# Kernel optimization log

Measured on AMD Instinct MI355X. Metric: run time of the kernel, lower is better.

## Reference

```python
import jax, jax.numpy as jnp
import numpy as np
from jax import lax

T, B, I, H = 512, 64, 1024, 1024
FORGET_BIAS = 1.0


def setup_inputs() -> dict:
    key = jax.random.key(0)
    k1, k2, k3 = jax.random.split(key, 3)
    x = jax.random.normal(k1, (T, B, I), dtype=jnp.float32)
    # xavier-ish init for kernel, scaled normal for recurrent kernel
    kernel = jax.random.normal(k2, (I, 4 * H), dtype=jnp.float32) * (1.0 / np.sqrt(I))
    recurrent_kernel = jax.random.normal(k3, (H, 4 * H), dtype=jnp.float32) * (1.0 / np.sqrt(H))
    bias = jnp.zeros((4 * H,), dtype=jnp.float32)
    bias = bias.at[2 * H:3 * H].set(FORGET_BIAS)  # forget gate bias (haste gate order i,g,f,o)
    return {"x": x, "kernel": kernel, "recurrent_kernel": recurrent_kernel, "bias": bias}


def reference(x, kernel, recurrent_kernel, bias):
    # x: [T, B, I]; haste LSTM, gate order (i, g, f, o); zoneout=0, dropout=0
    t, b, _ = x.shape
    h = recurrent_kernel.shape[0]
    # precompute input projection for all timesteps: [T, B, 4H]
    wx = jnp.einsum('tbi,ij->tbj', x, kernel) + bias

    def step(carry, wx_t):
        h_prev, c_prev = carry
        v = wx_t + h_prev @ recurrent_kernel  # [B, 4H]
        i_g, g_g, f_g, o_g = jnp.split(v, 4, axis=-1)
        i = jax.nn.sigmoid(i_g)
        g = jnp.tanh(g_g)
        f = jax.nn.sigmoid(f_g)
        o = jax.nn.sigmoid(o_g)
        c_new = f * c_prev + i * g
        h_new = o * jnp.tanh(c_new)
        return (h_new, c_new), h_new

    h0 = jnp.zeros((b, h), dtype=x.dtype)
    c0 = jnp.zeros((b, h), dtype=x.dtype)
    (h_last, c_last), output = lax.scan(step, (h0, c0), wx)
    # output: [T, B, H]; state: ([1,B,H], [1,B,H]) matching torch module
    return output, h_last[None], c_last[None]
```

## Files before the change

kernel.cpp:

```cpp
#include <hip/hip_runtime.h>
#include <math.h>

#define T_STEPS 512
#define B_SZ    64
#define I_SZ    1024
#define H_SZ    1024

__device__ __forceinline__ float sigmoidf_(float x) { return 1.0f / (1.0f + expf(-x)); }

#define BM 64
#define BN 128
#define BK 16

__global__ __launch_bounds__(256)
void wx_gemm(const float* __restrict__ X, const float* __restrict__ W,
             const float* __restrict__ bias, float* __restrict__ wx)
{
    __shared__ float As[BK][BM + 4];
    __shared__ float Bs[BK][BN];

    const int tid = threadIdx.x;
    const int tx  = tid & 15;
    const int ty  = tid >> 4;
    const int m0  = blockIdx.y * BM;
    const int n0  = blockIdx.x * BN;

    float acc[4][8] = {};

    const int arow = tid >> 2;
    const int ak   = (tid & 3) * 4;
    const int brow = tid >> 5;
    const int bcol = (tid & 31) * 4;

    const float* Ag = X + (size_t)(m0 + arow) * I_SZ + ak;
    const float* Bg = W + (size_t)brow * 4096 + n0 + bcol;

    for (int k0 = 0; k0 < I_SZ; k0 += BK) {
        float4 av  = *(const float4*)(Ag + k0);
        float4 bv0 = *(const float4*)(Bg + (size_t)k0 * 4096);
        float4 bv1 = *(const float4*)(Bg + (size_t)(k0 + 8) * 4096);
        __syncthreads();
        As[ak + 0][arow] = av.x;
        As[ak + 1][arow] = av.y;
        As[ak + 2][arow] = av.z;
        As[ak + 3][arow] = av.w;
        *(float4*)&Bs[brow][bcol]     = bv0;
        *(float4*)&Bs[brow + 8][bcol] = bv1;
        __syncthreads();
        #pragma unroll
        for (int kk = 0; kk < BK; ++kk) {
            float4 a  = *(const float4*)&As[kk][ty * 4];
            float4 b0 = *(const float4*)&Bs[kk][tx * 8];
            float4 b1 = *(const float4*)&Bs[kk][tx * 8 + 4];
            float aa[4] = {a.x, a.y, a.z, a.w};
            float bb[8] = {b0.x, b0.y, b0.z, b0.w, b1.x, b1.y, b1.z, b1.w};
            #pragma unroll
            for (int i = 0; i < 4; ++i)
                #pragma unroll
                for (int jn = 0; jn < 8; ++jn)
                    acc[i][jn] = fmaf(aa[i], bb[jn], acc[i][jn]);
        }
    }

    float4 bi0 = *(const float4*)(bias + n0 + tx * 8);
    float4 bi1 = *(const float4*)(bias + n0 + tx * 8 + 4);
    float bb[8] = {bi0.x, bi0.y, bi0.z, bi0.w, bi1.x, bi1.y, bi1.z, bi1.w};
    #pragma unroll
    for (int i = 0; i < 4; ++i) {
        float* orow = wx + (size_t)(m0 + ty * 4 + i) * 4096 + n0 + tx * 8;
        float4 s0 = make_float4(acc[i][0] + bb[0], acc[i][1] + bb[1],
                                acc[i][2] + bb[2], acc[i][3] + bb[3]);
        float4 s1 = make_float4(acc[i][4] + bb[4], acc[i][5] + bb[5],
                                acc[i][6] + bb[6], acc[i][7] + bb[7]);
        *(float4*)orow       = s0;
        *(float4*)(orow + 4) = s1;
    }
}

__device__ __forceinline__ void accum_tile(
    const float* __restrict__ vec,
    const float* __restrict__ mat,
    int j0, int tid, int b, int jj,
    float (&vs)[64][66], float (&ms)[64][20],
    float& a0, float& a1, float& a2, float& a3)
{
    const int lb  = tid & 63;
    const int lkq = tid >> 6;
    const int rk  = tid & 63;
    const int rg  = tid >> 6;

    const float* Vg = vec + (size_t)lb * 1024 + lkq * 16;
    const float* Mg = mat + (size_t)rk * 4096 + (size_t)rg * 1024 + j0;

    for (int k0 = 0; k0 < 1024; k0 += 64) {
        float4 v0 = *(const float4*)(Vg + k0 + 0);
        float4 v1 = *(const float4*)(Vg + k0 + 4);
        float4 v2 = *(const float4*)(Vg + k0 + 8);
        float4 v3 = *(const float4*)(Vg + k0 + 12);
        float4 mv = *(const float4*)(Mg + (size_t)k0 * 4096);
        __syncthreads();
        const int kb = lkq * 16;
        vs[kb +  0][lb] = v0.x; vs[kb +  1][lb] = v0.y;
        vs[kb +  2][lb] = v0.z; vs[kb +  3][lb] = v0.w;
        vs[kb +  4][lb] = v1.x; vs[kb +  5][lb] = v1.y;
        vs[kb +  6][lb] = v1.z; vs[kb +  7][lb] = v1.w;
        vs[kb +  8][lb] = v2.x; vs[kb +  9][lb] = v2.y;
        vs[kb + 10][lb] = v2.z; vs[kb + 11][lb] = v2.w;
        vs[kb + 12][lb] = v3.x; vs[kb + 13][lb] = v3.y;
        vs[kb + 14][lb] = v3.z; vs[kb + 15][lb] = v3.w;
        ms[rk][ 0 + rg] = mv.x;
        ms[rk][ 4 + rg] = mv.y;
        ms[rk][ 8 + rg] = mv.z;
        ms[rk][12 + rg] = mv.w;
        __syncthreads();
        #pragma unroll
        for (int kk = 0; kk < 64; ++kk) {
            float hv = vs[kk][b];
            float4 r = *(const float4*)&ms[kk][jj * 4];
            a0 = fmaf(hv, r.x, a0);
            a1 = fmaf(hv, r.y, a1);
            a2 = fmaf(hv, r.z, a2);
            a3 = fmaf(hv, r.w, a3);
        }
    }
}

__global__ __launch_bounds__(256)
void lstm_step(const float* __restrict__ wx_t,
               const float* __restrict__ x_t,
               const float* __restrict__ W,
               const float* __restrict__ bias,
               const float* __restrict__ h_prev,
               const float* __restrict__ R,
               float* __restrict__ h_out,
               float* __restrict__ c_st)
{
    __shared__ float vs[64][66];
    __shared__ float ms[64][20];

    const int tid = threadIdx.x;
    const int b   = tid & 63;
    const int jj  = tid >> 6;
    const int j0  = blockIdx.x * 4;
    const int j   = j0 + jj;

    float a0 = 0.f, a1 = 0.f, a2 = 0.f, a3 = 0.f;

    if (!wx_t) {
        accum_tile(x_t, W, j0, tid, b, jj, vs, ms, a0, a1, a2, a3);
        a0 += bias[j];
        a1 += bias[1024 + j];
        a2 += bias[2048 + j];
        a3 += bias[3072 + j];
    }
    if (h_prev)
        accum_tile(h_prev, R, j0, tid, b, jj, vs, ms, a0, a1, a2, a3);
    if (wx_t) {
        const float* wr = wx_t + (size_t)b * 4096 + j;
        a0 += wr[0];
        a1 += wr[1024];
        a2 += wr[2048];
        a3 += wr[3072];
    }

    const float ig = sigmoidf_(a0);
    const float gg = tanhf(a1);
    const float fg = sigmoidf_(a2);
    const float og = sigmoidf_(a3);
    const float cp = h_prev ? c_st[(size_t)b * 1024 + j] : 0.0f;
    const float cn = fg * cp + ig * gg;
    const float hn = og * tanhf(cn);
    c_st[(size_t)b * 1024 + j] = cn;

    __syncthreads();
    ((float*)vs)[b * 4 + jj] = hn;
    __syncthreads();
    if (tid < 64) {
        float4 v = *(const float4*)&((float*)vs)[tid * 4];
        *(float4*)&h_out[(size_t)tid * 1024 + j0] = v;
    }
}

__global__ __launch_bounds__(256)
void finalize(float* __restrict__ out, const float* __restrict__ c)
{
    const int i = blockIdx.x * 256 + threadIdx.x;
    const size_t TBH = (size_t)T_STEPS * B_SZ * H_SZ;
    const size_t BH  = (size_t)B_SZ * H_SZ;
    out[TBH + i]      = out[TBH - BH + i];
    out[TBH + BH + i] = c[i];
}

extern "C" void kernel_launch(void* const* d_in, const int* in_sizes, int n_in,
                              void* d_out, int out_size, void* d_ws, size_t ws_size,
                              hipStream_t stream)
{
    const float* x    = (const float*)d_in[0];
    const float* W    = (const float*)d_in[1];
    const float* R    = (const float*)d_in[2];
    const float* bias = (const float*)d_in[3];
    float* out = (float*)d_out;

    const size_t wx_elems = (size_t)T_STEPS * B_SZ * 4096;
    const bool have_ws = ws_size >= (wx_elems + (size_t)B_SZ * H_SZ) * sizeof(float);

    float* wx = (float*)d_ws;
    float* c  = have_ws ? (float*)d_ws + wx_elems : (float*)d_ws;

    if (have_ws) {
        dim3 grid(4096 / BN, (T_STEPS * B_SZ) / BM);
        wx_gemm<<<grid, 256, 0, stream>>>(x, W, bias, wx);
    }

    for (int t = 0; t < T_STEPS; ++t) {
        const float* wx_t = have_ws ? wx + (size_t)t * B_SZ * 4096 : nullptr;
        const float* x_t  = x + (size_t)t * B_SZ * I_SZ;
        const float* hp   = t ? out + (size_t)(t - 1) * B_SZ * H_SZ : nullptr;
        lstm_step<<<256, 256, 0, stream>>>(wx_t, x_t, W, bias, hp, R,
                                           out + (size_t)t * B_SZ * H_SZ, c);
    }

    finalize<<<256, 256, 0, stream>>>(out, c);
}
```

Measured before the change: 21.84 ms.

## Persistent LSTM scan kernel with grid barrier and split-bf16 MFMA recurrence

Replaces the 512 per-timestep kernel launches with a single persistent kernel of 256 blocks that synchronise through an atomic grid barrier. The recurrent matmul now runs on MFMA bf16 instructions, using a three-way bf16 split of both h and a pre-transposed R to approximate fp32 precision. Cell state stays in registers. The change targets launch overhead and the slow scalar FMA recurrence, at the cost of six MFMAs per product, a spin-barrier that depends on all 256 blocks being co-resident, and extra workspace.

Result: no change. 21.70 ms (-0.6%).

```diff
diff --git a/kernel.cpp b/kernel.cpp
--- a/kernel.cpp
+++ b/kernel.cpp
@@ -7,6 +7,18 @@
 #define H_SZ    1024
 
 __device__ __forceinline__ float sigmoidf_(float x) { return 1.0f / (1.0f + expf(-x)); }
+
+__device__ __forceinline__ short f2bf(float x) {
+    unsigned u = __float_as_uint(x);
+    unsigned r = (u + 0x7FFFu + ((u >> 16) & 1u)) >> 16;
+    return (short)r;
+}
+__device__ __forceinline__ float bf2f(short s) {
+    return __uint_as_float(((unsigned)(unsigned short)s) << 16);
+}
+
+typedef __attribute__((ext_vector_type(8))) short bf16x8;
+typedef __attribute__((ext_vector_type(4))) float f32x4;
 
 #define BM 64
 #define BN 128
@@ -77,9 +89,157 @@
     }
 }
 
+__global__ __launch_bounds__(256)
+void split_transpose_R(const float* __restrict__ R, short* __restrict__ Rh,
+                       short* __restrict__ Rm, short* __restrict__ Rl)
+{
+    __shared__ float tile[64][65];
+    const int tid = threadIdx.x;
+    const int n0 = blockIdx.x * 64;
+    const int k0 = blockIdx.y * 64;
+
+    #pragma unroll
+    for (int i = 0; i < 16; ++i) {
+        int kl = i * 4 + (tid >> 6);
+        tile[kl][tid & 63] = R[(size_t)(k0 + kl) * 4096 + n0 + (tid & 63)];
+    }
+    __syncthreads();
+    #pragma unroll
+    for (int i = 0; i < 16; ++i) {
+        int nl = i * 4 + (tid >> 6);
+        int kl = tid & 63;
+        float v = tile[kl][nl];
+        short sh = f2bf(v);
+        float r1 = v - bf2f(sh);
+        short sm = f2bf(r1);
+        float r2 = r1 - bf2f(sm);
+        short sl = f2bf(r2);
+        size_t o = (size_t)(n0 + nl) * 1024 + k0 + kl;
+        Rh[o] = sh; Rm[o] = sm; Rl[o] = sl;
+    }
+}
+
+__global__ __launch_bounds__(512, 2)
+void lstm_scan(const float* __restrict__ wx,
+               const short* __restrict__ Rh, const short* __restrict__ Rm,
+               const short* __restrict__ Rl,
+               short* hb,
+               float* __restrict__ out,
+               unsigned int* bar)
+{
+    __shared__ float red[8][4][16][16];
+
+    const int tid  = threadIdx.x;
+    const int w    = tid >> 6;
+    const int lane = tid & 63;
+    const int jg   = blockIdx.x & 63;
+    const int mt   = blockIdx.x >> 6;
+    const int b0   = mt * 16;
+    const int j0   = jg * 16;
+    const int frow = lane & 15;
+    const int quad = lane >> 4;
+    const int kbase = w * 128 + quad * 8;
+
+    const int m16 = tid >> 4;
+    const int n16 = tid & 15;
+    float c_state = 0.0f;
+
+    const size_t PLANE = 65536;
+
+    #pragma unroll 1
+    for (int t = 0; t < T_STEPS; ++t) {
+        const int pr = t & 1, pw = (t + 1) & 1;
+
+        float wxv0 = 0.f, wxv1 = 0.f, wxv2 = 0.f, wxv3 = 0.f;
+        if (tid < 256) {
+            const float* wp = wx + (size_t)t * 262144 + (size_t)(b0 + m16) * 4096 + j0 + n16;
+            wxv0 = wp[0]; wxv1 = wp[1024]; wxv2 = wp[2048]; wxv3 = wp[3072];
+        }
+
+        f32x4 acc0 = {0,0,0,0}, acc1 = {0,0,0,0}, acc2 = {0,0,0,0}, acc3 = {0,0,0,0};
+        if (t > 0) {
+            const short* hp = hb + (size_t)pr * 3 * PLANE + (size_t)(b0 + frow) * 1024;
+            #pragma unroll
+            for (int ki = 0; ki < 4; ++ki) {
+                const int ko = kbase + ki * 32;
+                bf16x8 ah = *(const bf16x8*)(hp + 0 * PLANE + ko);
+                bf16x8 am = *(const bf16x8*)(hp + 1 * PLANE + ko);
+                bf16x8 al = *(const bf16x8*)(hp + 2 * PLANE + ko);
+                #pragma unroll
+                for (int nt = 0; nt < 4; ++nt) {
+                    const size_t ro = (size_t)(nt * 1024 + j0 + frow) * 1024 + ko;
+                    bf16x8 bh = *(const bf16x8*)(Rh + ro);
+                    bf16x8 bm = *(const bf16x8*)(Rm + ro);
+                    bf16x8 bl = *(const bf16x8*)(Rl + ro);
+                    f32x4 a = (nt == 0) ? acc0 : (nt == 1) ? acc1 : (nt == 2) ? acc2 : acc3;
+                    a = __builtin_amdgcn_mfma_f32_16x16x32_bf16(ah, bh, a, 0, 0, 0);
+                    a = __builtin_amdgcn_mfma_f32_16x16x32_bf16(ah, bm, a, 0, 0, 0);
+                    a = __builtin_amdgcn_mfma_f32_16x16x32_bf16(am, bh, a, 0, 0, 0);
+                    a = __builtin_amdgcn_mfma_f32_16x16x32_bf16(ah, bl, a, 0, 0, 0);
+                    a = __builtin_amdgcn_mfma_f32_16x16x32_bf16(al, bh, a, 0, 0, 0);
+                    a = __builtin_amdgcn_mfma_f32_16x16x32_bf16(am, bm, a, 0, 0, 0);
+                    if (nt == 0) acc0 = a; else if (nt == 1) acc1 = a;
+                    else if (nt == 2) acc2 = a; else acc3 = a;
+                }
+            }
+        }
+
+        #pragma unroll
+        for (int r = 0; r < 4; ++r) {
+            red[w][0][quad * 4 + r][frow] = acc0[r];
+            red[w][1][quad * 4 + r][frow] = acc1[r];
+            red[w][2][quad * 4 + r][frow] = acc2[r];
+            red[w][3][quad * 4 + r][frow] = acc3[r];
+        }
+        __syncthreads();
+
+        if (tid < 256) {
+            float P0 = wxv0, P1 = wxv1, P2 = wxv2, P3 = wxv3;
+            #pragma unroll
+            for (int ww = 0; ww < 8; ++ww) {
+                P0 += red[ww][0][m16][n16];
+                P1 += red[ww][1][m16][n16];
+                P2 += red[ww][2][m16][n16];
+                P3 += red[ww][3][m16][n16];
+            }
+            const float ig = sigmoidf_(P0);
+            const float gg = tanhf(P1);
+            const float fg = sigmoidf_(P2);
+            const float og = sigmoidf_(P3);
+            c_state = fg * c_state + ig * gg;
+            const float hn = og * tanhf(c_state);
+
+            const size_t oidx = (size_t)(b0 + m16) * 1024 + (j0 + n16);
+            out[(size_t)t * 65536 + oidx] = hn;
+
+            short* hw = hb + (size_t)pw * 3 * PLANE + oidx;
+            short s0 = f2bf(hn);
+            float r1 = hn - bf2f(s0);
+            short s1 = f2bf(r1);
+            float r2 = r1 - bf2f(s1);
+            short s2 = f2bf(r2);
+            hw[0 * PLANE] = s0; hw[1 * PLANE] = s1; hw[2 * PLANE] = s2;
+
+            if (t == T_STEPS - 1) {
+                out[33554432 + oidx]         = hn;
+                out[33554432 + 65536 + oidx] = c_state;
+            }
+        }
+
+        __threadfence();
+        __syncthreads();
+        if (tid == 0) {
+            __hip_atomic_fetch_add(bar, 1u, __ATOMIC_RELEASE, __HIP_MEMORY_SCOPE_AGENT);
+            const unsigned target = 256u * (unsigned)(t + 1);
+            while (__hip_atomic_load(bar, __ATOMIC_ACQUIRE, __HIP_MEMORY_SCOPE_AGENT) < target)
+                __builtin_amdgcn_s_sleep(2);
+        }
+        __syncthreads();
+    }
+}
+
 __device__ __forceinline__ void accum_tile(
-    const float* __restrict__ vec,
-    const float* __restrict__ mat,
+    const float* __restrict__ vec, const float* __restrict__ mat,
     int j0, int tid, int b, int jj,
     float (&vs)[64][66], float (&ms)[64][20],
     float& a0, float& a1, float& a2, float& a3)
@@ -126,14 +286,10 @@
 }
 
 __global__ __launch_bounds__(256)
-void lstm_step(const float* __restrict__ wx_t,
-               const float* __restrict__ x_t,
-               const float* __restrict__ W,
-               const float* __restrict__ bias,
-               const float* __restrict__ h_prev,
-               const float* __restrict__ R,
-               float* __restrict__ h_out,
-               float* __restrict__ c_st)
+void lstm_step(const float* __restrict__ wx_t, const float* __restrict__ x_t,
+               const float* __restrict__ W, const float* __restrict__ bias,
+               const float* __restrict__ h_prev, const float* __restrict__ R,
+               float* __restrict__ h_out, float* __restrict__ c_st)
 {
     __shared__ float vs[64][66];
     __shared__ float ms[64][20];
@@ -201,9 +357,33 @@
     const float* bias = (const float*)d_in[3];
     float* out = (float*)d_out;
 
+    const size_t OFF_HB = 256;
+    const size_t OFF_RT = 786688;
+    const size_t OFF_WX = 25952512;
+    const size_t NEED_NEW = OFF_WX + (size_t)T_STEPS * B_SZ * 4096 * sizeof(float);
+
+    if (ws_size >= NEED_NEW) {
+        unsigned int* bar = (unsigned int*)d_ws;
+        short* hb  = (short*)((char*)d_ws + OFF_HB);
+        short* RTh = (short*)((char*)d_ws + OFF_RT);
+        short* RTm = (short*)((char*)d_ws + OFF_RT + 8388608);
+        short* RTl = (short*)((char*)d_ws + OFF_RT + 16777216);
+        float* wx  = (float*)((char*)d_ws + OFF_WX);
+
+        hipMemsetAsync(d_ws, 0, 256, stream);
+
+        dim3 tg(64, 16);
+        split_transpose_R<<<tg, 256, 0, stream>>>(R, RTh, RTm, RTl);
+
+        dim3 grid(4096 / BN, (T_STEPS * B_SZ) / BM);
+        wx_gemm<<<grid, 256, 0, stream>>>(x, W, bias, wx);
+
+        lstm_scan<<<256, 512, 0, stream>>>(wx, RTh, RTm, RTl, hb, out, bar);
+        return;
+    }
+
     const size_t wx_elems = (size_t)T_STEPS * B_SZ * 4096;
     const bool have_ws = ws_size >= (wx_elems + (size_t)B_SZ * H_SZ) * sizeof(float);
-
     float* wx = (float*)d_ws;
     float* c  = have_ws ? (float*)d_ws + wx_elems : (float*)d_ws;
 
@@ -211,7 +391,6 @@
         dim3 grid(4096 / BN, (T_STEPS * B_SZ) / BM);
         wx_gemm<<<grid, 256, 0, stream>>>(x, W, bias, wx);
     }
-
     for (int t = 0; t < T_STEPS; ++t) {
         const float* wx_t = have_ws ? wx + (size_t)t * B_SZ * 4096 : nullptr;
         const float* x_t  = x + (size_t)t * B_SZ * I_SZ;
@@ -219,6 +398,5 @@
         lstm_step<<<256, 256, 0, stream>>>(wx_t, x_t, W, bias, hp, R,
                                            out + (size_t)t * B_SZ * H_SZ, c);
     }
-
     finalize<<<256, 256, 0, stream>>>(out, c);
 }
```
